# Kernel optimization log

Hardware: AMD Instinct MI355X
Metric: run time of the kernel (lower is better)

The kernel has to match this reference:

```python
import jax, jax.numpy as jnp
import numpy as np
import math

B, T, E, H = 2, 2048, 1024, 16
HD = E // H
EPS = 1e-5


def rope(x):
    # x: [B,H,T,HD]. Faithful to source: cos/sin built from cat(freqs,freqs),
    # rotation uses interleaved pairing of even/odd channels.
    d = x.shape[-1]
    t = x.shape[-2]
    inv_freq = 1.0 / (10000.0 ** (jnp.arange(0, d, 2, dtype=jnp.float32) / d))
    freqs = jnp.arange(t, dtype=jnp.float32)[:, None] * inv_freq[None, :]  # [T, d/2]
    emb = jnp.concatenate([freqs, freqs], axis=-1)  # [T, d]
    cos = jnp.cos(emb)[None, None]  # [1,1,T,d]
    sin = jnp.sin(emb)[None, None]
    x1 = x[..., ::2]
    x2 = x[..., 1::2]
    x_rot = jnp.stack([-x2, x1], axis=-1).reshape(x.shape)
    return x * cos + x_rot * sin


def group_norm(y, w, b):
    # y: [B,T,E] -> normalize per (batch, head-group) over (HD, T) like torch GroupNorm on (B,E,T)
    yt = jnp.transpose(y, (0, 2, 1))  # [B,E,T]
    g = yt.reshape(B, H, HD * T)
    mu = jnp.mean(g, axis=-1, keepdims=True)
    var = jnp.var(g, axis=-1, keepdims=True)
    g = (g - mu) * jax.lax.rsqrt(var + EPS)
    yt = g.reshape(B, E, T) * w[None, :, None] + b[None, :, None]
    return jnp.transpose(yt, (0, 2, 1))


def setup_inputs() -> dict:
    key = jax.random.key(0)
    ks = jax.random.split(key, 13)
    s = 1.0 / math.sqrt(E)
    d = {"x": jax.random.normal(ks[0], (B, T, E), jnp.float32)}
    for i, n in enumerate(["q", "k", "v", "g", "o"]):
        d[f"W{n}"] = jax.random.uniform(ks[1 + 2 * i], (E, E), jnp.float32, -s, s)
        d[f"b{n}"] = jax.random.uniform(ks[2 + 2 * i], (E,), jnp.float32, -s, s)
    d["gn_w"] = jnp.ones((E,), jnp.float32)
    d["gn_b"] = jnp.zeros((E,), jnp.float32)
    return d


def reference(x, Wq, bq, Wk, bk, Wv, bv, Wg, bg, Wo, bo, gn_w, gn_b):
    scale = math.sqrt(HD)
    def proj(W, b):
        return (x @ W.T + b).reshape(B, T, H, HD).transpose(0, 2, 1, 3)  # [B,H,T,HD]
    Q = rope(proj(Wq, bq))
    K = rope(proj(Wk, bk))
    V = proj(Wv, bv)

    # decay mask exactly as in source: m=col idx, n=row idx; mask = (m>=n)*gamma^(m-n)
    gamma = 1.0 - 2.0 ** (-5.0 - jnp.arange(H, dtype=jnp.float32))  # [H]
    m = jnp.arange(T)[None, :]
    n = jnp.arange(T)[:, None]
    diff = (m - n).astype(jnp.float32)  # [T,T]
    mask = jnp.where(m >= n, gamma[:, None, None] ** diff[None], 0.0)  # [H,T,T]

    scores = jnp.einsum("bhid,bhjd->bhij", Q, K) / scale
    scores = scores * mask[None]
    out = jnp.einsum("bhij,bhjd->bhid", scores, V)  # [B,H,T,HD]
    out = out.transpose(0, 2, 1, 3).reshape(B, T, E)
    out = group_norm(out, gn_w, gn_b)
    gate = jax.nn.silu(x @ Wg.T + bg)
    return (gate * out) @ Wo.T + bo
```

## Files before the change

kernel.cpp:

```cpp
#include <hip/hip_runtime.h>
#include <math.h>

typedef unsigned short u16;
typedef unsigned int u32;
typedef __attribute__((ext_vector_type(8))) short short8;
typedef __attribute__((ext_vector_type(4))) float f32x4;

#define BB 2
#define TT 2048
#define EE 1024
#define HH 16
#define HDD 64
#define NC 32
#define CS 64

__device__ __forceinline__ float bf2f(u16 u){ union{unsigned i; float f;} v; v.i=((unsigned)u)<<16; return v.f; }
__device__ __forceinline__ u16 f2bf(float f){ union{float f; unsigned i;} v; v.f=f; return (u16)((v.i + 0x7fffu + ((v.i>>16)&1u))>>16); }

__device__ __forceinline__ void gload16(const void* g, void* l){
    __builtin_amdgcn_global_load_lds((const __attribute__((address_space(1))) void*)g,
                                     (__attribute__((address_space(3))) void*)l, 16, 0, 0);
}

__global__ __launch_bounds__(256)
void cvt_swz(const float* __restrict__ s0, const float* __restrict__ s1,
             const float* __restrict__ s2, const float* __restrict__ s3,
             const float* __restrict__ s4, const float* __restrict__ s5,
             u16* __restrict__ d0, u16* __restrict__ d1, u16* __restrict__ d2,
             u16* __restrict__ d3, u16* __restrict__ d4, u16* __restrict__ d5)
{
    const float* S; u16* D; int nch;
    switch (blockIdx.z) {
        case 0: S=s0; D=d0; nch=4096*128; break;
        case 1: S=s1; D=d1; nch=1024*128; break;
        case 2: S=s2; D=d2; nch=1024*128; break;
        case 3: S=s3; D=d3; nch=1024*128; break;
        case 4: S=s4; D=d4; nch=1024*128; break;
        default:S=s5; D=d5; nch=1024*128; break;
    }
    int ci = blockIdx.x*256 + threadIdx.x;
    if (ci >= nch) return;
    int r = ci >> 7, c = ci & 127;
    int pc = (c & ~3) | ((c & 3) ^ ((r >> 1) & 3));
    const float4* sp = (const float4*)(S + (size_t)r*EE + c*8);
    float4 f0 = sp[0], f1 = sp[1];
    short8 ov; u16* o = (u16*)&ov;
    o[0]=f2bf(f0.x); o[1]=f2bf(f0.y); o[2]=f2bf(f0.z); o[3]=f2bf(f0.w);
    o[4]=f2bf(f1.x); o[5]=f2bf(f1.y); o[6]=f2bf(f1.z); o[7]=f2bf(f1.w);
    *(short8*)(D + (size_t)r*EE + pc*8) = ov;
}

__global__ __launch_bounds__(256)
void trig_tab(float* __restrict__ ctab, float* __restrict__ stab)
{
    int idx = blockIdx.x*256 + threadIdx.x;
    int t = idx >> 5, f = idx & 31;
    float ang = (float)t * exp2f(-(float)f * (13.287712379549449f/32.f));
    ctab[idx] = cosf(ang);
    stab[idx] = sinf(ang);
}

__device__ __forceinline__ void gemm_core(const u16* __restrict__ A, const u16* __restrict__ Bm,
                                          u16* As, u16* Bs, int bm, int bn, f32x4 (&acc)[4][4])
{
    const int tid = threadIdx.x;
    const int lane = tid & 63;
    const int g = lane >> 4, rl = lane & 15;
    const int w = tid >> 6, wr = w >> 1, wc = w & 1;
    for (int k0 = 0; k0 < EE; k0 += 32) {
        __syncthreads();
        {
            int cc = tid, r = cc >> 2, c = cc & 3;
            gload16(A  + (size_t)(bm + r)*EE + k0 + c*8, &As[cc*8]);
            gload16(Bm + (size_t)(bn + r)*EE + k0 + c*8, &Bs[cc*8]);
            cc = tid + 256; r = cc >> 2; c = cc & 3;
            gload16(A  + (size_t)(bm + r)*EE + k0 + c*8, &As[cc*8]);
            gload16(Bm + (size_t)(bn + r)*EE + k0 + c*8, &Bs[cc*8]);
        }
        __syncthreads();
        short8 a[4], b[4];
        #pragma unroll
        for (int i = 0; i < 4; ++i) {
            int m = wr*64 + i*16 + rl;
            a[i] = *(const short8*)&As[m*32 + ((g ^ ((m>>1)&3)) << 3)];
            int n = wc*64 + i*16 + rl;
            b[i] = *(const short8*)&Bs[n*32 + ((g ^ ((n>>1)&3)) << 3)];
        }
        #pragma unroll
        for (int i = 0; i < 4; ++i)
            #pragma unroll
            for (int j = 0; j < 4; ++j)
                acc[i][j] = __builtin_amdgcn_mfma_f32_16x16x32_bf16(a[i], b[j], acc[i][j], 0, 0, 0);
    }
}

__global__ __launch_bounds__(256)
void gemm_qkvg(const u16* __restrict__ A,
               const u16* __restrict__ W0, const u16* __restrict__ W1,
               const u16* __restrict__ W2, const u16* __restrict__ W3,
               const float* __restrict__ b0, const float* __restrict__ b1,
               const float* __restrict__ b2, const float* __restrict__ b3,
               u16* __restrict__ C0, u16* __restrict__ C1,
               u16* __restrict__ C2, u16* __restrict__ C3)
{
    __shared__ u16 As[128*32], Bs[128*32];
    const u16* W; const float* bias; u16* C; int swz;
    switch (blockIdx.z) {
        case 0: W=W0; bias=b0; C=C0; swz=1; break;
        case 1: W=W1; bias=b1; C=C1; swz=1; break;
        case 2: W=W2; bias=b2; C=C2; swz=0; break;
        default:W=W3; bias=b3; C=C3; swz=0; break;
    }
    int bm = blockIdx.y*128, bn = blockIdx.x*128;
    f32x4 acc[4][4] = {};
    gemm_core(A, W, As, Bs, bm, bn, acc);
    const int lane = threadIdx.x & 63, g = lane>>4, rl = lane&15;
    const int w = threadIdx.x >> 6, wr = w>>1, wc = w&1;
    float bj[4];
    #pragma unroll
    for (int j = 0; j < 4; ++j) bj[j] = bias[bn + wc*64 + j*16 + rl];
    #pragma unroll
    for (int i = 0; i < 4; ++i)
      #pragma unroll
      for (int rr = 0; rr < 4; ++rr) {
        int m = bm + wr*64 + i*16 + g*4 + rr;
        #pragma unroll
        for (int j = 0; j < 4; ++j) {
            int n = bn + wc*64 + j*16 + rl;
            float v = acc[i][j][rr] + bj[j];
            int col = swz ? ((n & ~63) | ((((n>>3)&7) ^ (m&7)) << 3) | (n & 7)) : n;
            C[(size_t)m*EE + col] = f2bf(v);
        }
      }
}

__global__ __launch_bounds__(256)
void gemm_out(const u16* __restrict__ A, const u16* __restrict__ W,
              const float* __restrict__ bias, float* __restrict__ C)
{
    __shared__ u16 As[128*32], Bs[128*32];
    int bm = blockIdx.y*128, bn = blockIdx.x*128;
    f32x4 acc[4][4] = {};
    gemm_core(A, W, As, Bs, bm, bn, acc);
    const int lane = threadIdx.x & 63, g = lane>>4, rl = lane&15;
    const int w = threadIdx.x >> 6, wr = w>>1, wc = w&1;
    float bj[4];
    #pragma unroll
    for (int j = 0; j < 4; ++j) bj[j] = bias[bn + wc*64 + j*16 + rl];
    #pragma unroll
    for (int i = 0; i < 4; ++i)
      #pragma unroll
      for (int rr = 0; rr < 4; ++rr) {
        int m = bm + wr*64 + i*16 + g*4 + rr;
        #pragma unroll
        for (int j = 0; j < 4; ++j) {
            int n = bn + wc*64 + j*16 + rl;
            C[(size_t)m*EE + n] = acc[i][j][rr] + bj[j];
        }
      }
}

__global__ __launch_bounds__(256)
void rope_swz(u16* __restrict__ Q, u16* __restrict__ K,
              const float* __restrict__ ctab, const float* __restrict__ stab)
{
    u16* X = blockIdx.z ? K : Q;
    int ci = blockIdx.x*256 + threadIdx.x;
    int row = ci >> 7;
    int t = row & (TT-1);
    int c = ci & 127, h = c >> 3, p = c & 7;
    int d0 = (p ^ (t & 7)) << 3;
    u16* ptr = X + (size_t)row*EE + h*HDD + p*8;
    short8 xv = *(short8*)ptr;
    u16* xu = (u16*)&xv;
    const float* cr = ctab + t*32;
    const float* sr = stab + t*32;
    short8 ov; u16* o = (u16*)&ov;
    #pragma unroll
    for (int q = 0; q < 4; ++q) {
        int j0 = d0 + 2*q;
        float xe = bf2f(xu[2*q]), xo = bf2f(xu[2*q+1]);
        float c0 = cr[j0 & 31],     s0 = sr[j0 & 31];
        float c1 = cr[(j0+1) & 31], s1 = sr[(j0+1) & 31];
        o[2*q]   = f2bf(xe*c0 - xo*s0);
        o[2*q+1] = f2bf(xo*c1 + xe*s1);
    }
    *(short8*)ptr = ov;
}

__global__ __launch_bounds__(256)
void transV(const u16* __restrict__ V, u16* __restrict__ VT)
{
    __shared__ u16 ts[64*64];
    int t0 = blockIdx.x * 64, h = blockIdx.y, b = blockIdx.z;
    int tid = threadIdx.x;
    #pragma unroll
    for (int rr = 0; rr < 2; ++rr) {
        int cc = tid + rr*256;
        int r = cc >> 3, c = cc & 7;
        short8 v = *(const short8*)(V + (size_t)(b*TT + t0 + r)*EE + h*HDD + c*8);
        *(short8*)&ts[r*64 + ((c ^ (r & 7)) << 3)] = v;
    }
    __syncthreads();
    #pragma unroll
    for (int rr = 0; rr < 2; ++rr) {
        int oc = tid + rr*256;
        int d = oc & 63, tp = oc >> 6;
        short8 ov; u16* o = (u16*)&ov;
        #pragma unroll
        for (int e = 0; e < 8; ++e) {
            int t = tp*8 + e;
            o[e] = ts[t*64 + (((d>>3) ^ (t & 7)) << 3) + (d & 7)];
        }
        int ptp = tp ^ (d & 7);
        *(short8*)(VT + ((size_t)((b*HH + h)*HDD + d))*TT + t0 + ptp*8) = ov;
    }
}

__global__ __launch_bounds__(256)
void transK(const u16* __restrict__ K, u16* __restrict__ KT)
{
    __shared__ u16 ts[64*64];
    int t0 = blockIdx.x * 64, h = blockIdx.y, b = blockIdx.z;
    int tid = threadIdx.x;
    const float l2g = log2f(1.f - exp2f(-5.f - (float)h));
    #pragma unroll
    for (int rr = 0; rr < 2; ++rr) {
        int cc = tid + rr*256;
        int r = cc >> 3, c = cc & 7;
        short8 v = *(const short8*)(K + (size_t)(b*TT + t0 + r)*EE + h*HDD + c*8);
        *(short8*)&ts[r*64 + (c << 3)] = v;
    }
    __syncthreads();
    #pragma unroll
    for (int rr = 0; rr < 2; ++rr) {
        int oc = tid + rr*256;
        int d = oc & 63, tp = oc >> 6;
        short8 ov; u16* o = (u16*)&ov;
        #pragma unroll
        for (int e = 0; e < 8; ++e) {
            int t = tp*8 + e;
            float val = bf2f(ts[t*64 + (((d>>3) ^ (t & 7)) << 3) + (d & 7)]);
            o[e] = f2bf(val * exp2f(l2g * (float)t));
        }
        int ptp = tp ^ (d & 7);
        *(short8*)(KT + ((size_t)((b*HH + h)*HDD + d))*TT + t0 + ptp*8) = ov;
    }
}

__global__ __launch_bounds__(256)
void chunk_state(const u16* __restrict__ KT, const u16* __restrict__ VT,
                 float* __restrict__ Tb)
{
    __shared__ u16 Ks[64*64], Vs[64*64];
    const int tid = threadIdx.x, w = tid >> 6, lane = tid & 63;
    const int g = lane >> 4, rl = lane & 15;
    const int c = blockIdx.x, h = blockIdx.y, b = blockIdx.z;
    const int t0 = c*64;
    const size_t rowb = (size_t)((b*HH + h)*HDD);
    {
        int cc = tid, r = cc >> 3, ch = cc & 7;
        gload16(KT + (rowb + r)*TT + t0 + ch*8, &Ks[cc*8]);
        gload16(VT + (rowb + r)*TT + t0 + ch*8, &Vs[cc*8]);
        cc = tid + 256; r = cc >> 3; ch = cc & 7;
        gload16(KT + (rowb + r)*TT + t0 + ch*8, &Ks[cc*8]);
        gload16(VT + (rowb + r)*TT + t0 + ch*8, &Vs[cc*8]);
    }
    __syncthreads();
    int d2r = w*16 + rl;
    short8 af0 = *(const short8*)&Vs[d2r*64 + ((g ^ (d2r & 7)) << 3)];
    short8 af1 = *(const short8*)&Vs[d2r*64 + (((4+g) ^ (d2r & 7)) << 3)];
    f32x4 acc[4] = {};
    #pragma unroll
    for (int j = 0; j < 4; ++j) {
        int d1r = j*16 + rl;
        short8 b0 = *(const short8*)&Ks[d1r*64 + ((g ^ (d1r & 7)) << 3)];
        short8 b1 = *(const short8*)&Ks[d1r*64 + (((4+g) ^ (d1r & 7)) << 3)];
        acc[j] = __builtin_amdgcn_mfma_f32_16x16x32_bf16(af0, b0, acc[j], 0, 0, 0);
        acc[j] = __builtin_amdgcn_mfma_f32_16x16x32_bf16(af1, b1, acc[j], 0, 0, 0);
    }
    float* tb = Tb + ((size_t)((b*HH + h)*NC + c))*4096;
    #pragma unroll
    for (int j = 0; j < 4; ++j)
        #pragma unroll
        for (int rr = 0; rr < 4; ++rr)
            tb[(w*16 + g*4 + rr)*64 + j*16 + rl] = acc[j][rr];
}

__global__ __launch_bounds__(256)
void suffix_scan(const float* __restrict__ Tb, u16* __restrict__ Zb)
{
    __shared__ float lds[NC*512];
    const int q = blockIdx.x & 7;
    const int h = (blockIdx.x >> 3) & 15;
    const int b = blockIdx.x >> 7;
    const float l2g = log2f(1.f - exp2f(-5.f - (float)h));
    const float g64 = exp2f(l2g * 64.f);
    const float* tb = Tb + ((size_t)((b*HH + h)*NC))*4096 + q*512;
    u16* zb = Zb + ((size_t)((b*HH + h)*NC))*4096;
    const int tid = threadIdx.x;
    #pragma unroll
    for (int k = 0; k < 16; ++k) {
        int i4 = tid + k*256;
        int c = i4 >> 7, r = i4 & 127;
        *(float4*)&lds[c*512 + r*4] = *(const float4*)(tb + (size_t)c*4096 + r*4);
    }
    __syncthreads();
    int e0 = tid*2;
    int d2l = e0 >> 6, d1 = e0 & 63;
    int d2 = q*8 + d2l;
    int pos = d2*64 + (((d1>>3) ^ (d2 & 7)) << 3) + (d1 & 7);
    *(u32*)(zb + (size_t)31*4096 + pos) = 0u;
    float z0 = 0.f, z1 = 0.f;
    for (int c = 30; c >= 0; --c) {
        z0 = lds[(c+1)*512 + e0]     + g64*z0;
        z1 = lds[(c+1)*512 + e0 + 1] + g64*z1;
        u32 pk = (u32)f2bf(z0) | ((u32)f2bf(z1) << 16);
        *(u32*)(zb + (size_t)c*4096 + pos) = pk;
    }
}

__global__ __launch_bounds__(256)
void ret_out(const u16* __restrict__ Q, const u16* __restrict__ K,
             const u16* __restrict__ VT, const u16* __restrict__ Zb,
             float* __restrict__ R)
{
    __shared__ u16 Qs[64*64], Ks[64*64], Vs[64*64], Zs[64*64], Ss[64*64];
    const int tid = threadIdx.x, w = tid >> 6, lane = tid & 63;
    const int g = lane >> 4, rl = lane & 15;
    const int c = blockIdx.x, h = blockIdx.y, b = blockIdx.z;
    const int m0 = c*64;
    const float l2g = log2f(1.f - exp2f(-5.f - (float)h));
    const size_t vrow = (size_t)((b*HH + h)*HDD);
    const u16* zc = Zb + ((size_t)((b*HH + h)*NC + c))*4096;
    {
        int cc = tid, r = cc >> 3, ch = cc & 7;
        gload16(Q  + (size_t)(b*TT + m0 + r)*EE + h*HDD + ch*8, &Qs[cc*8]);
        gload16(K  + (size_t)(b*TT + m0 + r)*EE + h*HDD + ch*8, &Ks[cc*8]);
        gload16(VT + (vrow + r)*TT + m0 + ch*8, &Vs[cc*8]);
        gload16(zc + cc*8, &Zs[cc*8]);
        cc = tid + 256; r = cc >> 3; ch = cc & 7;
        gload16(Q  + (size_t)(b*TT + m0 + r)*EE + h*HDD + ch*8, &Qs[cc*8]);
        gload16(K  + (size_t)(b*TT + m0 + r)*EE + h*HDD + ch*8, &Ks[cc*8]);
        gload16(VT + (vrow + r)*TT + m0 + ch*8, &Vs[cc*8]);
        gload16(zc + cc*8, &Zs[cc*8]);
    }
    __syncthreads();
    const int mr = w*16 + rl;
    short8 qf[2];
    qf[0] = *(const short8*)&Qs[mr*64 + ((g ^ (rl & 7)) << 3)];
    qf[1] = *(const short8*)&Qs[mr*64 + (((4+g) ^ (rl & 7)) << 3)];
    f32x4 sacc[4] = {};
    #pragma unroll
    for (int j = 0; j < 4; ++j) {
        int n = j*16 + rl;
        short8 k0 = *(const short8*)&Ks[n*64 + ((g ^ (n & 7)) << 3)];
        short8 k1 = *(const short8*)&Ks[n*64 + (((4+g) ^ (n & 7)) << 3)];
        sacc[j] = __builtin_amdgcn_mfma_f32_16x16x32_bf16(qf[0], k0, sacc[j], 0, 0, 0);
        sacc[j] = __builtin_amdgcn_mfma_f32_16x16x32_bf16(qf[1], k1, sacc[j], 0, 0, 0);
    }
    float pn[4], pmv[4];
    #pragma unroll
    for (int j = 0; j < 4; ++j) pn[j] = exp2f(l2g * (float)(j*16 + rl));
    #pragma unroll
    for (int rr = 0; rr < 4; ++rr) pmv[rr] = exp2f(-l2g * (float)(w*16 + g*4 + rr));
    #pragma unroll
    for (int j = 0; j < 4; ++j) {
        int nl = j*16 + rl;
        #pragma unroll
        for (int rr = 0; rr < 4; ++rr) {
            int ml = w*16 + g*4 + rr;
            float wgt = (nl >= ml) ? 0.125f * pn[j] * pmv[rr] : 0.f;
            Ss[ml*64 + (((nl>>3) ^ (ml & 7)) << 3) + (nl & 7)] = f2bf(sacc[j][rr] * wgt);
        }
    }
    asm volatile("s_waitcnt lgkmcnt(0)" ::: "memory");
    f32x4 oacc[4] = {}, zacc[4] = {};
    #pragma unroll
    for (int s = 0; s < 2; ++s) {
        short8 sf = *(const short8*)&Ss[mr*64 + (((s*4 + g) ^ (rl & 7)) << 3)];
        #pragma unroll
        for (int j = 0; j < 4; ++j) {
            int d = j*16 + rl;
            short8 vf = *(const short8*)&Vs[d*64 + (((s*4 + g) ^ (d & 7)) << 3)];
            oacc[j] = __builtin_amdgcn_mfma_f32_16x16x32_bf16(sf, vf, oacc[j], 0, 0, 0);
            short8 zf = *(const short8*)&Zs[d*64 + (((s*4 + g) ^ (d & 7)) << 3)];
            zacc[j] = __builtin_amdgcn_mfma_f32_16x16x32_bf16(qf[s], zf, zacc[j], 0, 0, 0);
        }
    }
    const float g64 = exp2f(l2g * 64.f);
    #pragma unroll
    for (int j = 0; j < 4; ++j)
        #pragma unroll
        for (int rr = 0; rr < 4; ++rr) {
            int m_g = m0 + w*16 + g*4 + rr;
            float rs = 0.125f * g64 * pmv[rr];
            R[(size_t)(b*TT + m_g)*EE + h*HDD + j*16 + rl] = oacc[j][rr] + rs*zacc[j][rr];
        }
}

__global__ __launch_bounds__(256)
void gn_partial(const float* __restrict__ R, float* __restrict__ part)
{
    int bid = blockIdx.x;
    int bh = bid >> 4, seg = bid & 15;
    int b = bh >> 4, h = bh & 15;
    const float* base = R + (size_t)(b*TT + seg*128)*EE + h*HDD;
    float s = 0.f, sq = 0.f;
    #pragma unroll
    for (int k = 0; k < 8; ++k) {
        int i4 = threadIdx.x + 256*k;
        int t = i4 >> 4, dq = i4 & 15;
        float4 v = *(const float4*)(base + (size_t)t*EE + dq*4);
        s  += v.x + v.y + v.z + v.w;
        sq += v.x*v.x + v.y*v.y + v.z*v.z + v.w*v.w;
    }
    #pragma unroll
    for (int off = 32; off; off >>= 1) { s += __shfl_down(s, off, 64); sq += __shfl_down(sq, off, 64); }
    __shared__ float ls[4], lq[4];
    int lane = threadIdx.x & 63, wv = threadIdx.x >> 6;
    if (lane == 0) { ls[wv] = s; lq[wv] = sq; }
    __syncthreads();
    if (threadIdx.x == 0) {
        part[2*bid]   = ls[0]+ls[1]+ls[2]+ls[3];
        part[2*bid+1] = lq[0]+lq[1]+lq[2]+lq[3];
    }
}

__global__ void gn_finalize(const float* __restrict__ part, float* __restrict__ stats)
{
    int bh = threadIdx.x;
    if (bh < 32) {
        float s = 0.f, sq = 0.f;
        #pragma unroll
        for (int k = 0; k < 16; ++k) { s += part[2*(bh*16+k)]; sq += part[2*(bh*16+k)+1]; }
        const float inv = 1.f / (float)(TT*HDD);
        float mu = s * inv;
        float var = sq * inv - mu*mu;
        stats[2*bh]   = mu;
        stats[2*bh+1] = rsqrtf(var + 1e-5f);
    }
}

__global__ __launch_bounds__(256)
void zgate(const u16* __restrict__ G, const float* __restrict__ R,
           const float* __restrict__ stats, const float* __restrict__ gw,
           const float* __restrict__ gb, u16* __restrict__ Z)
{
    int ci = blockIdx.x*256 + threadIdx.x;
    int row = ci >> 7;
    int c = ci & 127;
    int e0 = c*8;
    int b = row >> 11;
    int bh = b*HH + (e0 >> 6);
    float mu = stats[2*bh], rs = stats[2*bh+1];
    short8 gv = *(const short8*)(G + (size_t)row*EE + e0);
    const u16* gu = (const u16*)&gv;
    const float* rp = R + (size_t)row*EE + e0;
    float4 r0 = *(const float4*)rp, r1 = *(const float4*)(rp+4);
    float rr[8] = {r0.x,r0.y,r0.z,r0.w,r1.x,r1.y,r1.z,r1.w};
    short8 ov; u16* o = (u16*)&ov;
    #pragma unroll
    for (int q = 0; q < 8; ++q) {
        float gvf = bf2f(gu[q]);
        float gate = gvf / (1.f + __expf(-gvf));
        float nv = (rr[q] - mu)*rs*gw[e0+q] + gb[e0+q];
        o[q] = f2bf(gate*nv);
    }
    int pc = (c & ~3) | ((c & 3) ^ ((row >> 1) & 3));
    *(short8*)(Z + (size_t)row*EE + pc*8) = ov;
}

extern "C" void kernel_launch(void* const* d_in, const int* in_sizes, int n_in,
                              void* d_out, int out_size, void* d_ws, size_t ws_size,
                              hipStream_t stream)
{
    const float* x  = (const float*)d_in[0];
    const float* Wq = (const float*)d_in[1];
    const float* bq = (const float*)d_in[2];
    const float* Wk = (const float*)d_in[3];
    const float* bk = (const float*)d_in[4];
    const float* Wv = (const float*)d_in[5];
    const float* bv = (const float*)d_in[6];
    const float* Wg = (const float*)d_in[7];
    const float* bg = (const float*)d_in[8];
    const float* Wo = (const float*)d_in[9];
    const float* bo = (const float*)d_in[10];
    const float* gw = (const float*)d_in[11];
    const float* gb = (const float*)d_in[12];
    float* out = (float*)d_out;

    char* p = (char*)d_ws;
    u16* xb  = (u16*)p;              p += (size_t)8<<20;
    u16* Wqb = (u16*)p;              p += (size_t)2<<20;
    u16* Wkb = (u16*)p;              p += (size_t)2<<20;
    u16* Wvb = (u16*)p;              p += (size_t)2<<20;
    u16* Wgb = (u16*)p;              p += (size_t)2<<20;
    u16* Wob = (u16*)p;              p += (size_t)2<<20;
    u16* Qb  = (u16*)p;              p += (size_t)8<<20;
    u16* Kb  = (u16*)p;              p += (size_t)8<<20;
    u16* Vb  = (u16*)p;              p += (size_t)8<<20;
    u16* Gb  = (u16*)p;              p += (size_t)8<<20;
    u16* VTb = (u16*)p;              p += (size_t)8<<20;
    u16* KTb = (u16*)p;              p += (size_t)8<<20;
    float* TbRb  = (float*)p;        p += (size_t)16<<20;
    float* part  = (float*)p;        p += 4096;
    float* stats = (float*)p;        p += 256;
    float* ctab  = (float*)p;        p += (size_t)65536*4;
    float* stab  = (float*)p;        p += (size_t)65536*4;
    u16* Zbuf = xb;
    float* Tb = TbRb;
    float* Rb = TbRb;
    u16* ZGb = xb;

    cvt_swz<<<dim3(2048,1,6), 256, 0, stream>>>(x, Wq, Wk, Wv, Wg, Wo,
                                                xb, Wqb, Wkb, Wvb, Wgb, Wob);
    trig_tab<<<256, 256, 0, stream>>>(ctab, stab);
    gemm_qkvg<<<dim3(8,32,4), 256, 0, stream>>>(xb, Wqb, Wkb, Wvb, Wgb,
                                                bq, bk, bv, bg, Qb, Kb, Vb, Gb);
    rope_swz<<<dim3(2048,1,2), 256, 0, stream>>>(Qb, Kb, ctab, stab);
    transV<<<dim3(32,16,2), 256, 0, stream>>>(Vb, VTb);
    transK<<<dim3(32,16,2), 256, 0, stream>>>(Kb, KTb);
    chunk_state<<<dim3(32,16,2), 256, 0, stream>>>(KTb, VTb, Tb);
    suffix_scan<<<256, 256, 0, stream>>>(Tb, Zbuf);
    ret_out<<<dim3(32,16,2), 256, 0, stream>>>(Qb, Kb, VTb, Zbuf, Rb);
    gn_partial<<<512, 256, 0, stream>>>(Rb, part);
    gn_finalize<<<1, 64, 0, stream>>>(part, stats);
    zgate<<<2048, 256, 0, stream>>>(Gb, Rb, stats, gw, gb, ZGb);
    gemm_out<<<dim3(8,32,1), 256, 0, stream>>>(ZGb, Wob, bo, out);
}
```

Before: 230.4 us.

## Triple-buffer GEMM k-loop with async LDS loads and enlarge QKVG tile to 256x256

Both projection GEMMs now use a three-slot shared-memory ring filled by global_load_lds, issuing loads two k-steps ahead and waiting with vmcnt so that one barrier per step replaces two. The fused QKVG GEMM also moves to 256x256 tiles with 512 threads and 8x4 MFMA accumulators per wave, which raises reuse of each loaded tile. The grid shrinks from 1024 to 256 blocks, and with more LDS and registers per block this may lower occupancy and leave some CUs underused.

```diff
diff --git a/kernel.cpp b/kernel.cpp
--- a/kernel.cpp
+++ b/kernel.cpp
@@ -60,41 +60,7 @@
     stab[idx] = sinf(ang);
 }
 
-__device__ __forceinline__ void gemm_core(const u16* __restrict__ A, const u16* __restrict__ Bm,
-                                          u16* As, u16* Bs, int bm, int bn, f32x4 (&acc)[4][4])
-{
-    const int tid = threadIdx.x;
-    const int lane = tid & 63;
-    const int g = lane >> 4, rl = lane & 15;
-    const int w = tid >> 6, wr = w >> 1, wc = w & 1;
-    for (int k0 = 0; k0 < EE; k0 += 32) {
-        __syncthreads();
-        {
-            int cc = tid, r = cc >> 2, c = cc & 3;
-            gload16(A  + (size_t)(bm + r)*EE + k0 + c*8, &As[cc*8]);
-            gload16(Bm + (size_t)(bn + r)*EE + k0 + c*8, &Bs[cc*8]);
-            cc = tid + 256; r = cc >> 2; c = cc & 3;
-            gload16(A  + (size_t)(bm + r)*EE + k0 + c*8, &As[cc*8]);
-            gload16(Bm + (size_t)(bn + r)*EE + k0 + c*8, &Bs[cc*8]);
-        }
-        __syncthreads();
-        short8 a[4], b[4];
-        #pragma unroll
-        for (int i = 0; i < 4; ++i) {
-            int m = wr*64 + i*16 + rl;
-            a[i] = *(const short8*)&As[m*32 + ((g ^ ((m>>1)&3)) << 3)];
-            int n = wc*64 + i*16 + rl;
-            b[i] = *(const short8*)&Bs[n*32 + ((g ^ ((n>>1)&3)) << 3)];
-        }
-        #pragma unroll
-        for (int i = 0; i < 4; ++i)
-            #pragma unroll
-            for (int j = 0; j < 4; ++j)
-                acc[i][j] = __builtin_amdgcn_mfma_f32_16x16x32_bf16(a[i], b[j], acc[i][j], 0, 0, 0);
-    }
-}
-
-__global__ __launch_bounds__(256)
+__global__ __launch_bounds__(512)
 void gemm_qkvg(const u16* __restrict__ A,
                const u16* __restrict__ W0, const u16* __restrict__ W1,
                const u16* __restrict__ W2, const u16* __restrict__ W3,
@@ -103,7 +69,8 @@
                u16* __restrict__ C0, u16* __restrict__ C1,
                u16* __restrict__ C2, u16* __restrict__ C3)
 {
-    __shared__ u16 As[128*32], Bs[128*32];
+    __shared__ u16 SA[3][256*32];
+    __shared__ u16 SB[3][256*32];
     const u16* W; const float* bias; u16* C; int swz;
     switch (blockIdx.z) {
         case 0: W=W0; bias=b0; C=C0; swz=1; break;
@@ -111,19 +78,61 @@
         case 2: W=W2; bias=b2; C=C2; swz=0; break;
         default:W=W3; bias=b3; C=C3; swz=0; break;
     }
-    int bm = blockIdx.y*128, bn = blockIdx.x*128;
-    f32x4 acc[4][4] = {};
-    gemm_core(A, W, As, Bs, bm, bn, acc);
-    const int lane = threadIdx.x & 63, g = lane>>4, rl = lane&15;
-    const int w = threadIdx.x >> 6, wr = w>>1, wc = w&1;
+    const int bm = blockIdx.y*256, bn = blockIdx.x*256;
+    const int tid = threadIdx.x;
+    const int lane = tid & 63, g = lane >> 4, rl = lane & 15;
+    const int w = tid >> 6, wr = w >> 2, wc = w & 3;
+
+    auto STAGE = [&](int slot, int kt) {
+        int k0 = kt*32;
+        #pragma unroll
+        for (int r2 = 0; r2 < 2; ++r2) {
+            int cc = tid + 512*r2;
+            int row = cc >> 2, ch = cc & 3;
+            gload16(A + (size_t)(bm + row)*EE + k0 + ch*8, &SA[slot][cc*8]);
+        }
+        #pragma unroll
+        for (int r2 = 0; r2 < 2; ++r2) {
+            int cc = tid + 512*r2;
+            int row = cc >> 2, ch = cc & 3;
+            gload16(W + (size_t)(bn + row)*EE + k0 + ch*8, &SB[slot][cc*8]);
+        }
+    };
+
+    f32x4 acc[8][4] = {};
+    STAGE(0, 0); STAGE(1, 1);
+    for (int t = 0; t < 32; ++t) {
+        if (t < 31) asm volatile("s_waitcnt vmcnt(4)" ::: "memory");
+        else        asm volatile("s_waitcnt vmcnt(0)" ::: "memory");
+        __builtin_amdgcn_s_barrier();
+        int cur = t % 3;
+        if (t + 2 < 32) STAGE((t+2) % 3, t+2);
+        const u16* SAc = SA[cur]; const u16* SBc = SB[cur];
+        short8 a[8], b[4];
+        #pragma unroll
+        for (int i = 0; i < 8; ++i) {
+            int m = wr*128 + i*16 + rl;
+            a[i] = *(const short8*)&SAc[m*32 + ((g ^ ((m>>1)&3)) << 3)];
+        }
+        #pragma unroll
+        for (int j = 0; j < 4; ++j) {
+            int n = wc*64 + j*16 + rl;
+            b[j] = *(const short8*)&SBc[n*32 + ((g ^ ((n>>1)&3)) << 3)];
+        }
+        #pragma unroll
+        for (int i = 0; i < 8; ++i)
+            #pragma unroll
+            for (int j = 0; j < 4; ++j)
+                acc[i][j] = __builtin_amdgcn_mfma_f32_16x16x32_bf16(a[i], b[j], acc[i][j], 0, 0, 0);
+    }
     float bj[4];
     #pragma unroll
     for (int j = 0; j < 4; ++j) bj[j] = bias[bn + wc*64 + j*16 + rl];
     #pragma unroll
-    for (int i = 0; i < 4; ++i)
+    for (int i = 0; i < 8; ++i)
       #pragma unroll
       for (int rr = 0; rr < 4; ++rr) {
-        int m = bm + wr*64 + i*16 + g*4 + rr;
+        int m = bm + wr*128 + i*16 + g*4 + rr;
         #pragma unroll
         for (int j = 0; j < 4; ++j) {
             int n = bn + wc*64 + j*16 + rl;
@@ -138,12 +147,52 @@
 void gemm_out(const u16* __restrict__ A, const u16* __restrict__ W,
               const float* __restrict__ bias, float* __restrict__ C)
 {
-    __shared__ u16 As[128*32], Bs[128*32];
-    int bm = blockIdx.y*128, bn = blockIdx.x*128;
+    __shared__ u16 SA[3][128*32];
+    __shared__ u16 SB[3][128*32];
+    const int bm = blockIdx.y*128, bn = blockIdx.x*128;
+    const int tid = threadIdx.x;
+    const int lane = tid & 63, g = lane >> 4, rl = lane & 15;
+    const int w = tid >> 6, wr = w >> 1, wc = w & 1;
+
+    auto STAGE = [&](int slot, int kt) {
+        int k0 = kt*32;
+        #pragma unroll
+        for (int r2 = 0; r2 < 2; ++r2) {
+            int cc = tid + 256*r2;
+            int row = cc >> 2, ch = cc & 3;
+            gload16(A + (size_t)(bm + row)*EE + k0 + ch*8, &SA[slot][cc*8]);
+        }
+        #pragma unroll
+        for (int r2 = 0; r2 < 2; ++r2) {
+            int cc = tid + 256*r2;
+            int row = cc >> 2, ch = cc & 3;
+            gload16(W + (size_t)(bn + row)*EE + k0 + ch*8, &SB[slot][cc*8]);
+        }
+    };
+
     f32x4 acc[4][4] = {};
-    gemm_core(A, W, As, Bs, bm, bn, acc);
-    const int lane = threadIdx.x & 63, g = lane>>4, rl = lane&15;
-    const int w = threadIdx.x >> 6, wr = w>>1, wc = w&1;
+    STAGE(0, 0); STAGE(1, 1);
+    for (int t = 0; t < 32; ++t) {
+        if (t < 31) asm volatile("s_waitcnt vmcnt(4)" ::: "memory");
+        else        asm volatile("s_waitcnt vmcnt(0)" ::: "memory");
+        __builtin_amdgcn_s_barrier();
+        int cur = t % 3;
+        if (t + 2 < 32) STAGE((t+2) % 3, t+2);
+        const u16* SAc = SA[cur]; const u16* SBc = SB[cur];
+        short8 a[4], b[4];
+        #pragma unroll
+        for (int i = 0; i < 4; ++i) {
+            int m = wr*64 + i*16 + rl;
+            a[i] = *(const short8*)&SAc[m*32 + ((g ^ ((m>>1)&3)) << 3)];
+            int n = wc*64 + i*16 + rl;
+            b[i] = *(const short8*)&SBc[n*32 + ((g ^ ((n>>1)&3)) << 3)];
+        }
+        #pragma unroll
+        for (int i = 0; i < 4; ++i)
+            #pragma unroll
+            for (int j = 0; j < 4; ++j)
+                acc[i][j] = __builtin_amdgcn_mfma_f32_16x16x32_bf16(a[i], b[j], acc[i][j], 0, 0, 0);
+    }
     float bj[4];
     #pragma unroll
     for (int j = 0; j < 4; ++j) bj[j] = bias[bn + wc*64 + j*16 + rl];
@@ -516,7 +565,7 @@
     cvt_swz<<<dim3(2048,1,6), 256, 0, stream>>>(x, Wq, Wk, Wv, Wg, Wo,
                                                 xb, Wqb, Wkb, Wvb, Wgb, Wob);
     trig_tab<<<256, 256, 0, stream>>>(ctab, stab);
-    gemm_qkvg<<<dim3(8,32,4), 256, 0, stream>>>(xb, Wqb, Wkb, Wvb, Wgb,
+    gemm_qkvg<<<dim3(4,16,4), 512, 0, stream>>>(xb, Wqb, Wkb, Wvb, Wgb,
                                                 bq, bk, bv, bg, Qb, Kb, Vb, Gb);
     rope_swz<<<dim3(2048,1,2), 256, 0, stream>>>(Qb, Kb, ctab, stab);
     transV<<<dim3(32,16,2), 256, 0, stream>>>(Vb, VTb);
```

After: 230.9 us. Within noise of the previous version (+0.2%).
